# Kernel tuning notes

Measured on AMD Instinct MI355X. Metric: run time of the kernel, lower is better.

## Reference

```python
import jax, jax.numpy as jnp
import numpy as np

STRIDE = 8
OUT = 96                 # feature map size fh = fw
SEARCH = OUT * STRIDE    # 768, search image size
RATIOS = [0.33, 0.5, 1.0, 2.0, 3.0]
SCALES = [4, 8, 16]
PRE_NMS = 1024
POST_NMS = 256
NMS_THRESH = 0.7


def _make_anchors():
    # anchor widths/heights per (ratio, scale), base size = stride * scale
    ws, hs = [], []
    for r in RATIOS:
        for s in SCALES:
            ws.append(STRIDE * s / np.sqrt(r))
            hs.append(STRIDE * s * np.sqrt(r))
    ws = np.asarray(ws, np.float32)  # [A]
    hs = np.asarray(hs, np.float32)
    ori = SEARCH // 2 - (OUT // 2) * STRIDE
    c = ori + STRIDE * np.arange(OUT, dtype=np.float32)
    cy, cx = np.meshgrid(c, c, indexing="ij")  # [OUT, OUT]
    x1 = cx[None] - ws[:, None, None] * 0.5  # [A, OUT, OUT]
    y1 = cy[None] - hs[:, None, None] * 0.5
    x2 = cx[None] + ws[:, None, None] * 0.5
    y2 = cy[None] + hs[:, None, None] * 0.5
    return np.stack([x1, y1, x2, y2], axis=-1).reshape(-1, 4)  # [A*K, 4]


def setup_inputs() -> dict:
    key = jax.random.key(0)
    k1, k2 = jax.random.split(key)
    pred_cls = jax.random.normal(k1, (32, 30, 96, 96), jnp.float32)
    pred_reg = jax.random.normal(k2, (32, 60, 96, 96), jnp.float32) * 0.2
    anchors = jnp.asarray(_make_anchors())
    return {"pred_cls": pred_cls, "pred_reg": pred_reg, "anchors": anchors}


def _nms_pad(boxes, scores):
    """boxes [N,4] sorted by score desc, scores [N]. Returns [POST_NMS,5] padded."""
    x1, y1, x2, y2 = boxes[:, 0], boxes[:, 1], boxes[:, 2], boxes[:, 3]
    areas = (x2 - x1 + 1.0) * (y2 - y1 + 1.0)
    ix1 = jnp.maximum(x1[:, None], x1[None, :])
    iy1 = jnp.maximum(y1[:, None], y1[None, :])
    ix2 = jnp.minimum(x2[:, None], x2[None, :])
    iy2 = jnp.minimum(y2[:, None], y2[None, :])
    inter = jnp.maximum(ix2 - ix1 + 1.0, 0.0) * jnp.maximum(iy2 - iy1 + 1.0, 0.0)
    iou = inter / (areas[:, None] + areas[None, :] - inter)
    n = boxes.shape[0]
    idxs = jnp.arange(n)

    def body(keep, i):
        sup = keep[i] & (iou[i] > NMS_THRESH) & (idxs > i)
        return keep & ~sup, None

    keep, _ = jax.lax.scan(body, jnp.ones((n,), bool), idxs)
    pos = jnp.cumsum(keep) - 1
    dst = jnp.where(keep & (pos < POST_NMS), pos, POST_NMS)  # pad row for dropped
    rows = jnp.concatenate([scores[:, None], boxes], axis=1)  # [N,5] score first
    out = jnp.zeros((POST_NMS + 1, 5), boxes.dtype).at[dst].set(rows)
    return out[:POST_NMS]


def reference(pred_cls, pred_reg, anchors):
    b, a2, h, w = pred_cls.shape
    A = a2 // 2
    # log-softmax over the 2-way fg/bg channel; take foreground log-probs
    logp = jax.nn.log_softmax(pred_cls.reshape(b, 2, A, h, w), axis=1)
    scores = logp[:, 1].reshape(b, -1)  # [b, A*h*w]
    # deltas: (b,4A,h,w) -> (b,4,A,h,w) -> (b,A,h,w,4) -> (b,A*h*w,4)
    deltas = pred_reg.reshape(b, 4, A, h, w).transpose(0, 2, 3, 4, 1).reshape(b, -1, 4)
    aw = anchors[:, 2] - anchors[:, 0] + 1.0
    ah = anchors[:, 3] - anchors[:, 1] + 1.0
    acx = anchors[:, 0] + 0.5 * aw
    acy = anchors[:, 1] + 0.5 * ah
    dx, dy, dw, dh = deltas[..., 0], deltas[..., 1], deltas[..., 2], deltas[..., 3]
    pcx = dx * aw + acx
    pcy = dy * ah + acy
    pw = jnp.exp(dw) * aw
    ph = jnp.exp(dh) * ah
    boxes = jnp.stack([pcx - 0.5 * pw, pcy - 0.5 * ph, pcx + 0.5 * pw, pcy + 0.5 * ph], axis=-1)
    boxes = jnp.clip(boxes, 0.0, SEARCH - 1.0)  # clip to image
    top_s, top_i = jax.lax.top_k(scores, PRE_NMS)  # per-image pre-NMS top-k
    top_b = jnp.take_along_axis(boxes, top_i[..., None], axis=1)  # [b,PRE,4]
    return jax.vmap(_nms_pad)(top_b, top_s)  # [b, POST_NMS, 5]
```

## Files before the change

kernel.cpp:

```cpp
#include <hip/hip_runtime.h>
#include <stdint.h>

#define NANCH 138240
#define NANCH4 34560
#define B_CNT 32
#define PRE 1024
#define POST 256
#define BINS 8192
#define CAP 4096
#define SBLK 15
#define SLICE4 2304
#define TLOC 192
#define LOCCAP 273
#define PAD_KEY 0xFFFFFFFFFFFFFFFFull

typedef unsigned long long u64;

__device__ __forceinline__ unsigned key32(float sc) {
    unsigned u = __float_as_uint(sc);
    unsigned s = (u & 0x80000000u) ? ~u : (u | 0x80000000u);
    return ~s;
}

__device__ __forceinline__ unsigned key_of(float x0, float x1) {
    float m  = fmaxf(x0, x1);
    float e0 = expf(x0 - m);
    float e1 = expf(x1 - m);
    float sc = (x1 - m) - logf(e0 + e1);
    return key32(sc);
}

__device__ __forceinline__ void decode_box(const float* __restrict__ reg,
                                           const float* __restrict__ anch,
                                           int b, int idx, float box[4]) {
    const float* rb = reg + (size_t)b * 4 * NANCH;
    float dx = rb[idx];
    float dy = rb[idx + NANCH];
    float dw = rb[idx + 2 * NANCH];
    float dh = rb[idx + 3 * NANCH];
    float ax1 = anch[idx * 4 + 0], ay1 = anch[idx * 4 + 1];
    float ax2 = anch[idx * 4 + 2], ay2 = anch[idx * 4 + 3];
    float aw  = __fadd_rn(__fsub_rn(ax2, ax1), 1.0f);
    float ah  = __fadd_rn(__fsub_rn(ay2, ay1), 1.0f);
    float acx = __fadd_rn(ax1, __fmul_rn(0.5f, aw));
    float acy = __fadd_rn(ay1, __fmul_rn(0.5f, ah));
    float pcx = __fadd_rn(__fmul_rn(dx, aw), acx);
    float pcy = __fadd_rn(__fmul_rn(dy, ah), acy);
    float pw  = __fmul_rn(expf(dw), aw);
    float ph  = __fmul_rn(expf(dh), ah);
    float hx  = __fmul_rn(0.5f, pw);
    float hy  = __fmul_rn(0.5f, ph);
    box[0] = fminf(fmaxf(__fsub_rn(pcx, hx), 0.0f), 767.0f);
    box[1] = fminf(fmaxf(__fsub_rn(pcy, hy), 0.0f), 767.0f);
    box[2] = fminf(fmaxf(__fadd_rn(pcx, hx), 0.0f), 767.0f);
    box[3] = fminf(fmaxf(__fadd_rn(pcy, hy), 0.0f), 767.0f);
}

__global__ __launch_bounds__(1024) void select_kernel(const float* __restrict__ cls,
                                                      u64* __restrict__ cand) {
    __shared__ unsigned h[BINS];
    __shared__ unsigned s_part[1024];
    __shared__ u64 loc[LOCCAP];
    __shared__ int s_b;
    __shared__ int lcnt;
    const int b = blockIdx.y;
    const int s = blockIdx.x;
    const int t = threadIdx.x;
    if (t == 0) lcnt = 0;
    for (int i = t; i < BINS; i += 1024) h[i] = 0;
    __syncthreads();

    const float4* cb4 = (const float4*)(cls + (size_t)b * 2 * NANCH);
    const int base4 = s * SLICE4;

    for (int k = 0; k < 3; ++k) {
        int off = k * 1024 + t;
        if (off < SLICE4) {
            int g4 = base4 + off;
            float4 a0 = cb4[g4];
            float4 a1 = cb4[g4 + NANCH4];
            atomicAdd(&h[key_of(a0.x, a1.x) >> 19], 1u);
            atomicAdd(&h[key_of(a0.y, a1.y) >> 19], 1u);
            atomicAdd(&h[key_of(a0.z, a1.z) >> 19], 1u);
            atomicAdd(&h[key_of(a0.w, a1.w) >> 19], 1u);
        }
    }
    __syncthreads();

    unsigned bin[8];
    unsigned seg = 0;
    #pragma unroll
    for (int i = 0; i < 8; ++i) { bin[i] = h[t * 8 + i]; seg += bin[i]; }
    s_part[t] = seg;
    __syncthreads();
    for (int off = 1; off < 1024; off <<= 1) {
        unsigned v = (t >= off) ? s_part[t - off] : 0u;
        __syncthreads();
        s_part[t] += v;
        __syncthreads();
    }
    unsigned incl = s_part[t];
    unsigned excl = incl - seg;
    if (incl >= TLOC && excl < TLOC) {
        unsigned cum = excl;
        int bs = t * 8 + 7;
        for (int i = 0; i < 8; ++i) {
            if (cum + bin[i] >= TLOC) { bs = t * 8 + i; break; }
            cum += bin[i];
        }
        s_b = bs;
    }
    __syncthreads();
    const int bs = s_b;

    for (int k = 0; k < 3; ++k) {
        int off = k * 1024 + t;
        if (off < SLICE4) {
            int g4 = base4 + off;
            float4 a0 = cb4[g4];
            float4 a1 = cb4[g4 + NANCH4];
            float x0[4] = {a0.x, a0.y, a0.z, a0.w};
            float x1[4] = {a1.x, a1.y, a1.z, a1.w};
            #pragma unroll
            for (int j = 0; j < 4; ++j) {
                unsigned key = key_of(x0[j], x1[j]);
                if ((int)(key >> 19) <= bs) {
                    int pos = atomicAdd(&lcnt, 1);
                    if (pos < LOCCAP)
                        loc[pos] = ((u64)key << 32) | (unsigned)(g4 * 4 + j);
                }
            }
        }
    }
    __syncthreads();
    int n = lcnt; if (n > LOCCAP) n = LOCCAP;
    u64* segp = cand + (size_t)b * CAP + s * LOCCAP;
    for (int i = t; i < LOCCAP; i += 1024)
        segp[i] = (i < n) ? loc[i] : PAD_KEY;
    if (s == 0 && t == 0) cand[(size_t)b * CAP + (CAP - 1)] = PAD_KEY;
}

__global__ __launch_bounds__(512) void lsort_kernel(u64* __restrict__ cand) {
    __shared__ u64 sb[1024];
    const int c = blockIdx.x;
    const int b = blockIdx.y;
    const int t = threadIdx.x;
    u64* seg = cand + (size_t)b * CAP + c * 1024;
    for (int i = t; i < 1024; i += 512) sb[i] = seg[i];
    __syncthreads();
    for (int k = 2; k <= 1024; k <<= 1) {
        for (int j = k >> 1; j > 0; j >>= 1) {
            int i  = ((t & ~(j - 1)) << 1) | (t & (j - 1));
            int p  = i | j;
            bool up = ((i & k) == 0);
            u64 a = sb[i], bb = sb[p];
            if ((a > bb) == up) { sb[i] = bb; sb[p] = a; }
            __syncthreads();
        }
    }
    for (int i = t; i < 1024; i += 512) seg[i] = sb[i];
}

__global__ __launch_bounds__(1024) void merge_kernel(const u64* __restrict__ cand,
                                                     const float* __restrict__ reg,
                                                     const float* __restrict__ anch,
                                                     float* __restrict__ topS,
                                                     float* __restrict__ topB) {
    __shared__ u64 runs[CAP];
    __shared__ u64 outk[PRE];
    const int b = blockIdx.x;
    const int t = threadIdx.x;
    for (int i = t; i < CAP; i += 1024) runs[i] = cand[(size_t)b * CAP + i];
    __syncthreads();

    #pragma unroll
    for (int r = 0; r < 4; ++r) {
        u64 x = runs[r * 1024 + t];
        int rank = t;
        #pragma unroll
        for (int q = 0; q < 4; ++q) {
            if (q == r) continue;
            const u64* run = &runs[q * 1024];
            int lo = 0, hi = 1024;
            while (lo < hi) {
                int mid = (lo + hi) >> 1;
                if (run[mid] < x) lo = mid + 1; else hi = mid;
            }
            rank += lo;
        }
        if (rank < PRE) outk[rank] = x;
    }
    __syncthreads();

    u64 key = outk[t];
    int idx = (int)(key & 0xFFFFFFFFu);
    unsigned ks = (unsigned)(key >> 32);
    unsigned s  = ~ks;
    unsigned u  = (s & 0x80000000u) ? (s & 0x7FFFFFFFu) : ~s;
    float sc = __uint_as_float(u);
    float box[4];
    decode_box(reg, anch, b, idx, box);
    topS[b * PRE + t] = sc;
    float* tb = topB + ((size_t)b * PRE + t) * 4;
    tb[0] = box[0]; tb[1] = box[1]; tb[2] = box[2]; tb[3] = box[3];
}

__global__ __launch_bounds__(1024) void mask_kernel(const float* __restrict__ topB,
                                                    u64* __restrict__ masks) {
    const int w = blockIdx.x;
    const int b = blockIdx.y;
    const int i = threadIdx.x;
    __shared__ float sx1[64], sy1[64], sx2[64], sy2[64], sar[64];
    if (i < 64) {
        const float* p = topB + ((size_t)b * PRE + w * 64 + i) * 4;
        float x1 = p[0], y1 = p[1], x2 = p[2], y2 = p[3];
        sx1[i] = x1; sy1[i] = y1; sx2[i] = x2; sy2[i] = y2;
        sar[i] = __fmul_rn(__fadd_rn(__fsub_rn(x2, x1), 1.0f),
                           __fadd_rn(__fsub_rn(y2, y1), 1.0f));
    }
    __syncthreads();
    const int jbase = w * 64;
    u64* dst = &masks[((size_t)b * PRE + i) * 16 + w];
    if (i >= jbase + 63) { *dst = 0ull; return; }
    const float* p = topB + ((size_t)b * PRE + i) * 4;
    float x1 = p[0], y1 = p[1], x2 = p[2], y2 = p[3];
    float ar = __fmul_rn(__fadd_rn(__fsub_rn(x2, x1), 1.0f),
                         __fadd_rn(__fsub_rn(y2, y1), 1.0f));
    u64 m = 0ull;
    for (int j = 0; j < 64; j++) {
        int jj = jbase + j;
        if (jj > i) {
            float ix1 = fmaxf(x1, sx1[j]);
            float iy1 = fmaxf(y1, sy1[j]);
            float ix2 = fminf(x2, sx2[j]);
            float iy2 = fminf(y2, sy2[j]);
            float iw = fmaxf(__fadd_rn(__fsub_rn(ix2, ix1), 1.0f), 0.0f);
            float ih = fmaxf(__fadd_rn(__fsub_rn(iy2, iy1), 1.0f), 0.0f);
            float inter = __fmul_rn(iw, ih);
            float denom = __fsub_rn(__fadd_rn(ar, sar[j]), inter);
            float iou = __fdiv_rn(inter, denom);
            if (iou > 0.7f) m |= (1ull << j);
        }
    }
    *dst = m;
}

__device__ __forceinline__ u64 shfl_xor_u64(u64 v, int lanemask) {
    int lo = __shfl_xor((int)(v & 0xFFFFFFFFull), lanemask);
    int hi = __shfl_xor((int)(v >> 32), lanemask);
    return ((u64)(unsigned)hi << 32) | (unsigned)lo;
}

__global__ __launch_bounds__(64) void nms_kernel(const u64* __restrict__ masks,
                                                 const float* __restrict__ topS,
                                                 const float* __restrict__ topB,
                                                 float* __restrict__ out) {
    const int b = blockIdx.x;
    const int t = threadIdx.x;
    __shared__ u64 rem[16];
    __shared__ int kept[POST];
    __shared__ int s_nk;
    if (t < 16) rem[t] = 0ull;
    __syncthreads();

    const u64* mb = masks + (size_t)b * PRE * 16;
    const int w = t >> 2, g = t & 3;
    int prefix = 0;

    u64 dv_cur = mb[(size_t)t * 16 + 0];
    u64 cw_cur[16];
    #pragma unroll
    for (int k = 0; k < 16; ++k)
        cw_cur[k] = mb[((size_t)(g * 16 + k)) * 16 + w];

    for (int c = 0; c < 16; ++c) {
        u64 dv_nxt = 0ull;
        u64 cw_nxt[16];
        if (c < 15) {
            const u64* nb = mb + (size_t)(c + 1) * 64 * 16;
            dv_nxt = nb[(size_t)t * 16 + (c + 1)];
            #pragma unroll
            for (int k = 0; k < 16; ++k)
                cw_nxt[k] = nb[((size_t)(g * 16 + k)) * 16 + w];
        } else {
            #pragma unroll
            for (int k = 0; k < 16; ++k) cw_nxt[k] = 0ull;
        }

        u64 alive = ~rem[c];
        int dlo = (int)(dv_cur & 0xFFFFFFFFull);
        int dhi = (int)(dv_cur >> 32);

        for (int l = 0; l < 64; ++l) {
            unsigned lo = (unsigned)__builtin_amdgcn_readlane(dlo, l);
            unsigned hi = (unsigned)__builtin_amdgcn_readlane(dhi, l);
            u64 dl = ((u64)hi << 32) | lo;
            u64 a = (alive >> l) & 1ull;
            alive &= ~(a ? dl : 0ull);
        }

        if ((alive >> t) & 1ull) {
            int pos = prefix + (int)__popcll(alive & ((1ull << t) - 1ull));
            if (pos < POST) kept[pos] = c * 64 + t;
        }
        prefix += (int)__popcll(alive);

        u64 acc = 0ull;
        #pragma unroll
        for (int k = 0; k < 16; ++k)
            if ((alive >> (g * 16 + k)) & 1ull) acc |= cw_cur[k];
        acc |= shfl_xor_u64(acc, 1);
        acc |= shfl_xor_u64(acc, 2);
        __syncthreads();
        if (g == 0 && w > c) rem[w] |= acc;
        __syncthreads();

        if (prefix >= POST) break;

        dv_cur = dv_nxt;
        #pragma unroll
        for (int k = 0; k < 16; ++k) cw_cur[k] = cw_nxt[k];
    }

    if (t == 0) s_nk = (prefix < POST) ? prefix : POST;
    __syncthreads();
    const int n = s_nk;

    float* ob = out + (size_t)b * POST * 5;
    for (int r = t; r < POST; r += 64) {
        if (r < n) {
            int i = kept[r];
            ob[r * 5 + 0] = topS[b * PRE + i];
            const float* tb = topB + ((size_t)b * PRE + i) * 4;
            ob[r * 5 + 1] = tb[0];
            ob[r * 5 + 2] = tb[1];
            ob[r * 5 + 3] = tb[2];
            ob[r * 5 + 4] = tb[3];
        } else {
            ob[r * 5 + 0] = 0.0f; ob[r * 5 + 1] = 0.0f; ob[r * 5 + 2] = 0.0f;
            ob[r * 5 + 3] = 0.0f; ob[r * 5 + 4] = 0.0f;
        }
    }
}

extern "C" void kernel_launch(void* const* d_in, const int* in_sizes, int n_in,
                              void* d_out, int out_size, void* d_ws, size_t ws_size,
                              hipStream_t stream) {
    const float* cls  = (const float*)d_in[0];
    const float* reg  = (const float*)d_in[1];
    const float* anch = (const float*)d_in[2];

    char* ws = (char*)d_ws;
    float* topS  = (float*)ws;
    float* topB  = (float*)(ws + 131072);
    u64*   cand  = (u64*)(ws + 655360);
    u64*   masks = (u64*)(ws + 1703936);

    select_kernel<<<dim3(SBLK, B_CNT), 1024, 0, stream>>>(cls, cand);
    lsort_kernel <<<dim3(4, B_CNT), 512, 0, stream>>>(cand);
    merge_kernel <<<B_CNT, 1024, 0, stream>>>(cand, reg, anch, topS, topB);
    mask_kernel  <<<dim3(16, B_CNT), 1024, 0, stream>>>(topB, masks);
    nms_kernel   <<<B_CNT, 64, 0, stream>>>(masks, topS, topB, (float*)d_out);
}
```

Before: 94.78 us.

## Drop full IoU mask kernel; compute diagonal masks in merge and lazy IoU in NMS

The separate mask kernel that built the full 1024x1024 IoU bitmask is removed. The merge kernel now computes only the 64x64 diagonal blocks, and the NMS kernel, now 1024 threads, computes IoU on demand between each chunk's surviving boxes and the next 1024 candidates, stopping once 256 boxes are kept. This removes a kernel launch and the IoU work and mask traffic for off-diagonal blocks that are never needed after early exit. The cost is serial per-chunk IoU work inside a single block per image, with a barrier for every chunk.

```diff
diff --git a/kernel.cpp b/kernel.cpp
--- a/kernel.cpp
+++ b/kernel.cpp
@@ -28,6 +28,19 @@
     float e1 = expf(x1 - m);
     float sc = (x1 - m) - logf(e0 + e1);
     return key32(sc);
+}
+
+__device__ __forceinline__ bool iou_gt(float x1, float y1, float x2, float y2, float ar,
+                                       float ox1, float oy1, float ox2, float oy2, float oar) {
+    float ix1 = fmaxf(x1, ox1);
+    float iy1 = fmaxf(y1, oy1);
+    float ix2 = fminf(x2, ox2);
+    float iy2 = fminf(y2, oy2);
+    float iw = fmaxf(__fadd_rn(__fsub_rn(ix2, ix1), 1.0f), 0.0f);
+    float ih = fmaxf(__fadd_rn(__fsub_rn(iy2, iy1), 1.0f), 0.0f);
+    float inter = __fmul_rn(iw, ih);
+    float denom = __fsub_rn(__fadd_rn(ar, oar), inter);
+    return __fdiv_rn(inter, denom) > 0.7f;
 }
 
 __device__ __forceinline__ void decode_box(const float* __restrict__ reg,
@@ -165,9 +178,11 @@
                                                      const float* __restrict__ reg,
                                                      const float* __restrict__ anch,
                                                      float* __restrict__ topS,
-                                                     float* __restrict__ topB) {
+                                                     float* __restrict__ topB,
+                                                     u64* __restrict__ diag) {
     __shared__ u64 runs[CAP];
     __shared__ u64 outk[PRE];
+    __shared__ float sx1[PRE], sy1[PRE], sx2[PRE], sy2[PRE], sar[PRE];
     const int b = blockIdx.x;
     const int t = threadIdx.x;
     for (int i = t; i < CAP; i += 1024) runs[i] = cand[(size_t)b * CAP + i];
@@ -203,139 +218,105 @@
     topS[b * PRE + t] = sc;
     float* tb = topB + ((size_t)b * PRE + t) * 4;
     tb[0] = box[0]; tb[1] = box[1]; tb[2] = box[2]; tb[3] = box[3];
-}
-
-__global__ __launch_bounds__(1024) void mask_kernel(const float* __restrict__ topB,
-                                                    u64* __restrict__ masks) {
-    const int w = blockIdx.x;
-    const int b = blockIdx.y;
-    const int i = threadIdx.x;
-    __shared__ float sx1[64], sy1[64], sx2[64], sy2[64], sar[64];
-    if (i < 64) {
-        const float* p = topB + ((size_t)b * PRE + w * 64 + i) * 4;
-        float x1 = p[0], y1 = p[1], x2 = p[2], y2 = p[3];
-        sx1[i] = x1; sy1[i] = y1; sx2[i] = x2; sy2[i] = y2;
-        sar[i] = __fmul_rn(__fadd_rn(__fsub_rn(x2, x1), 1.0f),
-                           __fadd_rn(__fsub_rn(y2, y1), 1.0f));
-    }
-    __syncthreads();
-    const int jbase = w * 64;
-    u64* dst = &masks[((size_t)b * PRE + i) * 16 + w];
-    if (i >= jbase + 63) { *dst = 0ull; return; }
-    const float* p = topB + ((size_t)b * PRE + i) * 4;
-    float x1 = p[0], y1 = p[1], x2 = p[2], y2 = p[3];
-    float ar = __fmul_rn(__fadd_rn(__fsub_rn(x2, x1), 1.0f),
-                         __fadd_rn(__fsub_rn(y2, y1), 1.0f));
+    sx1[t] = box[0]; sy1[t] = box[1]; sx2[t] = box[2]; sy2[t] = box[3];
+    sar[t] = __fmul_rn(__fadd_rn(__fsub_rn(box[2], box[0]), 1.0f),
+                       __fadd_rn(__fsub_rn(box[3], box[1]), 1.0f));
+    __syncthreads();
+
+    const int jbase = t & ~63;
+    float x1 = sx1[t], y1 = sy1[t], x2 = sx2[t], y2 = sy2[t], ar = sar[t];
     u64 m = 0ull;
-    for (int j = 0; j < 64; j++) {
+    for (int j = 0; j < 64; ++j) {
         int jj = jbase + j;
-        if (jj > i) {
-            float ix1 = fmaxf(x1, sx1[j]);
-            float iy1 = fmaxf(y1, sy1[j]);
-            float ix2 = fminf(x2, sx2[j]);
-            float iy2 = fminf(y2, sy2[j]);
-            float iw = fmaxf(__fadd_rn(__fsub_rn(ix2, ix1), 1.0f), 0.0f);
-            float ih = fmaxf(__fadd_rn(__fsub_rn(iy2, iy1), 1.0f), 0.0f);
-            float inter = __fmul_rn(iw, ih);
-            float denom = __fsub_rn(__fadd_rn(ar, sar[j]), inter);
-            float iou = __fdiv_rn(inter, denom);
-            if (iou > 0.7f) m |= (1ull << j);
-        }
-    }
-    *dst = m;
-}
-
-__device__ __forceinline__ u64 shfl_xor_u64(u64 v, int lanemask) {
-    int lo = __shfl_xor((int)(v & 0xFFFFFFFFull), lanemask);
-    int hi = __shfl_xor((int)(v >> 32), lanemask);
-    return ((u64)(unsigned)hi << 32) | (unsigned)lo;
-}
-
-__global__ __launch_bounds__(64) void nms_kernel(const u64* __restrict__ masks,
-                                                 const float* __restrict__ topS,
-                                                 const float* __restrict__ topB,
-                                                 float* __restrict__ out) {
+        if (jj > t && iou_gt(x1, y1, x2, y2, ar,
+                             sx1[jj], sy1[jj], sx2[jj], sy2[jj], sar[jj]))
+            m |= (1ull << j);
+    }
+    diag[(size_t)b * PRE + t] = m;
+}
+
+__global__ __launch_bounds__(1024) void nms_kernel(const u64* __restrict__ diag,
+                                                   const float* __restrict__ topS,
+                                                   const float* __restrict__ topB,
+                                                   float* __restrict__ out) {
+    __shared__ float sx1[PRE], sy1[PRE], sx2[PRE], sy2[PRE], sar[PRE];
+    __shared__ u64 rem[16];
+    __shared__ u64 alive_sh;
+    __shared__ int kept[POST];
+    __shared__ int s_prefix;
     const int b = blockIdx.x;
     const int t = threadIdx.x;
-    __shared__ u64 rem[16];
-    __shared__ int kept[POST];
-    __shared__ int s_nk;
+    const int lane = t & 63, wv = t >> 6;
+
+    float4 bx = ((const float4*)topB)[(size_t)b * PRE + t];
+    sx1[t] = bx.x; sy1[t] = bx.y; sx2[t] = bx.z; sy2[t] = bx.w;
+    sar[t] = __fmul_rn(__fadd_rn(__fsub_rn(bx.z, bx.x), 1.0f),
+                       __fadd_rn(__fsub_rn(bx.w, bx.y), 1.0f));
     if (t < 16) rem[t] = 0ull;
-    __syncthreads();
-
-    const u64* mb = masks + (size_t)b * PRE * 16;
-    const int w = t >> 2, g = t & 3;
-    int prefix = 0;
-
-    u64 dv_cur = mb[(size_t)t * 16 + 0];
-    u64 cw_cur[16];
-    #pragma unroll
-    for (int k = 0; k < 16; ++k)
-        cw_cur[k] = mb[((size_t)(g * 16 + k)) * 16 + w];
-
+    if (t == 0) s_prefix = 0;
+    __syncthreads();
+
+    int nfinal = 0;
     for (int c = 0; c < 16; ++c) {
-        u64 dv_nxt = 0ull;
-        u64 cw_nxt[16];
-        if (c < 15) {
-            const u64* nb = mb + (size_t)(c + 1) * 64 * 16;
-            dv_nxt = nb[(size_t)t * 16 + (c + 1)];
-            #pragma unroll
-            for (int k = 0; k < 16; ++k)
-                cw_nxt[k] = nb[((size_t)(g * 16 + k)) * 16 + w];
-        } else {
-            #pragma unroll
-            for (int k = 0; k < 16; ++k) cw_nxt[k] = 0ull;
-        }
-
-        u64 alive = ~rem[c];
-        int dlo = (int)(dv_cur & 0xFFFFFFFFull);
-        int dhi = (int)(dv_cur >> 32);
-
-        for (int l = 0; l < 64; ++l) {
-            unsigned lo = (unsigned)__builtin_amdgcn_readlane(dlo, l);
-            unsigned hi = (unsigned)__builtin_amdgcn_readlane(dhi, l);
-            u64 dl = ((u64)hi << 32) | lo;
-            u64 a = (alive >> l) & 1ull;
-            alive &= ~(a ? dl : 0ull);
-        }
-
-        if ((alive >> t) & 1ull) {
+        if (wv == 0) {
+            u64 dv = diag[(size_t)b * PRE + c * 64 + lane];
+            int dlo = (int)(dv & 0xFFFFFFFFull);
+            int dhi = (int)(dv >> 32);
+            u64 alive = ~rem[c];
+            for (int l = 0; l < 64; ++l) {
+                unsigned lo = (unsigned)__builtin_amdgcn_readlane(dlo, l);
+                unsigned hi = (unsigned)__builtin_amdgcn_readlane(dhi, l);
+                u64 dl = ((u64)hi << 32) | lo;
+                u64 a = (alive >> l) & 1ull;
+                alive &= ~(a ? dl : 0ull);
+            }
+            if (lane == 0) alive_sh = alive;
+        }
+        __syncthreads();
+        const u64 alive = alive_sh;
+        const int prefix = s_prefix;
+        const int newprefix = prefix + (int)__popcll(alive);
+
+        if (t < 64 && ((alive >> t) & 1ull)) {
             int pos = prefix + (int)__popcll(alive & ((1ull << t) - 1ull));
             if (pos < POST) kept[pos] = c * 64 + t;
         }
-        prefix += (int)__popcll(alive);
-
-        u64 acc = 0ull;
-        #pragma unroll
-        for (int k = 0; k < 16; ++k)
-            if ((alive >> (g * 16 + k)) & 1ull) acc |= cw_cur[k];
-        acc |= shfl_xor_u64(acc, 1);
-        acc |= shfl_xor_u64(acc, 2);
+
+        bool sup = false;
+        const int fr = (c + 1) * 64 + t;
+        if (fr < PRE && newprefix < POST) {
+            float fx1 = sx1[fr], fy1 = sy1[fr], fx2 = sx2[fr], fy2 = sy2[fr];
+            float far_ = sar[fr];
+            u64 al = alive;
+            while (al) {
+                int l = __ffsll((long long)al) - 1;
+                al &= al - 1ull;
+                int i = c * 64 + l;
+                if (iou_gt(sx1[i], sy1[i], sx2[i], sy2[i], sar[i],
+                           fx1, fy1, fx2, fy2, far_)) { sup = true; break; }
+            }
+        }
+        u64 bal = __ballot(sup);
+        if (lane == 0) {
+            int w = c + 1 + wv;
+            if (w < 16 && bal) rem[w] |= bal;
+        }
+        if (t == 0) s_prefix = newprefix;
         __syncthreads();
-        if (g == 0 && w > c) rem[w] |= acc;
-        __syncthreads();
-
-        if (prefix >= POST) break;
-
-        dv_cur = dv_nxt;
-        #pragma unroll
-        for (int k = 0; k < 16; ++k) cw_cur[k] = cw_nxt[k];
-    }
-
-    if (t == 0) s_nk = (prefix < POST) ? prefix : POST;
-    __syncthreads();
-    const int n = s_nk;
-
+        nfinal = newprefix;
+        if (newprefix >= POST) break;
+    }
+
+    const int n = (nfinal < POST) ? nfinal : POST;
     float* ob = out + (size_t)b * POST * 5;
-    for (int r = t; r < POST; r += 64) {
+    for (int r = t; r < POST; r += 1024) {
         if (r < n) {
             int i = kept[r];
             ob[r * 5 + 0] = topS[b * PRE + i];
-            const float* tb = topB + ((size_t)b * PRE + i) * 4;
-            ob[r * 5 + 1] = tb[0];
-            ob[r * 5 + 2] = tb[1];
-            ob[r * 5 + 3] = tb[2];
-            ob[r * 5 + 4] = tb[3];
+            ob[r * 5 + 1] = sx1[i];
+            ob[r * 5 + 2] = sy1[i];
+            ob[r * 5 + 3] = sx2[i];
+            ob[r * 5 + 4] = sy2[i];
         } else {
             ob[r * 5 + 0] = 0.0f; ob[r * 5 + 1] = 0.0f; ob[r * 5 + 2] = 0.0f;
             ob[r * 5 + 3] = 0.0f; ob[r * 5 + 4] = 0.0f;
@@ -354,11 +335,10 @@
     float* topS  = (float*)ws;
     float* topB  = (float*)(ws + 131072);
     u64*   cand  = (u64*)(ws + 655360);
-    u64*   masks = (u64*)(ws + 1703936);
+    u64*   diag  = (u64*)(ws + 1703936);
 
     select_kernel<<<dim3(SBLK, B_CNT), 1024, 0, stream>>>(cls, cand);
     lsort_kernel <<<dim3(4, B_CNT), 512, 0, stream>>>(cand);
-    merge_kernel <<<B_CNT, 1024, 0, stream>>>(cand, reg, anch, topS, topB);
-    mask_kernel  <<<dim3(16, B_CNT), 1024, 0, stream>>>(topB, masks);
-    nms_kernel   <<<B_CNT, 64, 0, stream>>>(masks, topS, topB, (float*)d_out);
-}
+    merge_kernel <<<B_CNT, 1024, 0, stream>>>(cand, reg, anch, topS, topB, diag);
+    nms_kernel   <<<B_CNT, 1024, 0, stream>>>(diag, topS, topB, (float*)d_out);
+}
```

Result: slower. 128.0 us (+35.0%).
